# Performance work log

Hardware: AMD Instinct MI355X
Metric: run time of the kernel (lower is better)

The kernel has to match this reference:

```python
import jax, jax.numpy as jnp
import numpy as np

# Config constants (match init_kwargs)
E = 16          # n_routed_experts
G = 4           # n_groups
TOPK_G = 2      # topk_groups
K = 4           # n_activated_experts
ROUTE_SCALE = 2.5446


def setup_inputs() -> dict:
    key = jax.random.key(0)
    ks = jax.random.split(key, 9)
    T, D, H = 2048, 1024, 704
    HS = 2 * H  # shared FFN hidden = n_shared_experts * expert_hidden_dim
    sc = lambda k, shape, fan_in: (jax.random.normal(k, shape, jnp.float32)
                                   * (fan_in ** -0.5))
    return {
        "x":      jax.random.normal(ks[0], (T, D), jnp.float32),
        "gate_w": sc(ks[1], (E, D), D),
        "gate_b": jnp.zeros((E,), jnp.float32),       # V3 routing bias (init 0)
        "w1":     sc(ks[2], (E, H, D), D),            # gate proj per expert
        "w3":     sc(ks[3], (E, H, D), D),            # up proj per expert
        "w2":     sc(ks[4], (E, D, H), H),            # down proj per expert
        "ws1":    sc(ks[5], (HS, D), D),              # shared FFN gate proj
        "ws3":    sc(ks[6], (HS, D), D),              # shared FFN up proj
        "ws2":    sc(ks[7], (D, HS), HS),             # shared FFN down proj
    }


def _gate(x, gate_w, gate_b):
    """DeepSeek-V3 sigmoid gate with bias routing + group-limited masking."""
    T = x.shape[0]
    logits = x @ gate_w.T                                   # [T, E]
    scores = jax.nn.sigmoid(logits).astype(jnp.float32)     # original_scores
    routing = scores + gate_b                               # bias only affects routing
    g = routing.reshape(T, G, E // G)
    # use_bias=True -> group score = sum of top-2 routing scores in group
    group_scores = jnp.sum(jax.lax.top_k(g, 2)[0], axis=-1)     # [T, G]
    top_groups = jax.lax.top_k(group_scores, TOPK_G)[1]         # [T, TOPK_G]
    keep = jnp.any(jnp.arange(G)[None, :, None] == top_groups[:, None, :],
                   axis=-1)                                     # [T, G]
    routing = jnp.where(keep[:, :, None], g, -jnp.inf).reshape(T, E)
    idx = jax.lax.top_k(routing, K)[1]                          # [T, K]
    w = jnp.take_along_axis(scores, idx, axis=1)                # un-biased weights
    w = w / jnp.clip(jnp.sum(w, axis=-1, keepdims=True), 1e-9)  # sigmoid renorm
    w = (w * ROUTE_SCALE).astype(x.dtype)
    return w, idx


def reference(x, gate_w, gate_b, w1, w3, w2, ws1, ws3, ws2):
    T, D = x.shape
    weights, idx = _gate(x, gate_w, gate_b)                 # [T,K], [T,K]
    # Dense dispatch/combine matrix: combine[t, e] = gate weight (0 if unrouted)
    combine = jnp.zeros((T, E), x.dtype).at[
        jnp.arange(T)[:, None], idx].add(weights)           # [T, E]
    # Routed experts: SwiGLU per expert, grouped GEMMs
    hg = jnp.einsum('td,ehd->eth', x, w1)                   # [E, T, H]
    hu = jnp.einsum('td,ehd->eth', x, w3)                   # [E, T, H]
    eo = jnp.einsum('eth,edh->etd', jax.nn.silu(hg) * hu, w2)  # [E, T, D]
    y_routed = jnp.einsum('etd,te->td', eo, combine)        # [T, D]
    # Shared experts (always active SwiGLU)
    y_shared = (jax.nn.silu(x @ ws1.T) * (x @ ws3.T)) @ ws2.T
    return y_routed + y_shared
```

## Files before the change

kernel.cpp:

```cpp
#include <hip/hip_runtime.h>
#include <hip/hip_bf16.h>
#include <math.h>

typedef __attribute__((ext_vector_type(4))) float   f32x4;
typedef __attribute__((ext_vector_type(8))) short   short8;
typedef __attribute__((ext_vector_type(8))) __bf16  bf16x8;

union SB8 { short8 s; bf16x8 b; };

__device__ __forceinline__ short f2bf(float f) {
  union { float f; unsigned u; } v; v.f = f;
  unsigned r = v.u + 0x7fffu + ((v.u >> 16) & 1u);
  return (short)(r >> 16);
}

__device__ __forceinline__ short8 cvt8(f32x4 a, f32x4 b) {
  short8 r;
  r[0] = f2bf(a[0]); r[1] = f2bf(a[1]); r[2] = f2bf(a[2]); r[3] = f2bf(a[3]);
  r[4] = f2bf(b[0]); r[5] = f2bf(b[1]); r[6] = f2bf(b[2]); r[7] = f2bf(b[3]);
  return r;
}

__device__ __forceinline__ void ldsload16(const short* g, short* l) {
  __builtin_amdgcn_global_load_lds(
      (const __attribute__((address_space(1))) unsigned int*)g,
      (__attribute__((address_space(3))) unsigned int*)l, 16, 0, 0);
}

#define TT   2048
#define DD   1024
#define HH   704
#define HSS  1408
#define EE   16
#define CAP  2048

#define O1  2097152ULL
#define O2  13631488ULL
#define O3  25165824ULL
#define O4  36700160ULL
#define O5  38141952ULL
#define O6  39583744ULL
#define CVT_TOTAL 41025536ULL
#define CVT_BLOCKS 5008

__global__ __launch_bounds__(256)
void cvt_gate(const float* __restrict__ x,  const float* __restrict__ w1,
              const float* __restrict__ w3, const float* __restrict__ w2,
              const float* __restrict__ s1, const float* __restrict__ s3,
              const float* __restrict__ s2, short* __restrict__ dst,
              const float* __restrict__ gw, const float* __restrict__ gb,
              int* __restrict__ counts, int* __restrict__ tok,
              float* __restrict__ wgt, int* __restrict__ eslot)
{
  if (blockIdx.x < CVT_BLOCKS) {
    const size_t blk = (size_t)blockIdx.x * 8192;
    #pragma unroll
    for (int k = 0; k < 4; k++) {
      size_t i = blk + (size_t)k * 2048 + (size_t)threadIdx.x * 8;
      const float* src;
      if      (i < O1) src = x  + i;
      else if (i < O2) src = w1 + (i - O1);
      else if (i < O3) src = w3 + (i - O2);
      else if (i < O4) src = w2 + (i - O3);
      else if (i < O5) src = s1 + (i - O4);
      else if (i < O6) src = s3 + (i - O5);
      else             src = s2 + (i - O6);
      f32x4 a = *(const f32x4*)src;
      f32x4 b = *(const f32x4*)(src + 4);
      *(short8*)(dst + i) = cvt8(a, b);
    }
    return;
  }

  const int lane = threadIdx.x & 63;
  const int wid  = threadIdx.x >> 6;
  const int t    = (blockIdx.x - CVT_BLOCKS) * 4 + wid;
  const int e    = lane & 15;
  const int p    = lane >> 4;

  const float* xp = x + (size_t)t * DD + p * 256;
  const float* gp = gw + (size_t)e * DD + p * 256;

  double acc = 0.0;
  #pragma unroll 8
  for (int i = 0; i < 64; i++) {
    f32x4 xa = *(const f32x4*)(xp + i * 4);
    f32x4 ga = *(const f32x4*)(gp + i * 4);
    acc += (double)xa[0] * (double)ga[0];
    acc += (double)xa[1] * (double)ga[1];
    acc += (double)xa[2] * (double)ga[2];
    acc += (double)xa[3] * (double)ga[3];
  }
  acc += __shfl_xor(acc, 16);
  acc += __shfl_xor(acc, 32);
  float accf = (float)acc;

  float lf[EE], sc[EE], r[EE];
  #pragma unroll
  for (int j = 0; j < EE; j++) lf[j] = __shfl(accf, j);
  #pragma unroll
  for (int j = 0; j < EE; j++) {
    sc[j] = 1.f / (1.f + expf(-lf[j]));
    r[j] = sc[j] + gb[j];
  }
  float gs[4];
  #pragma unroll
  for (int g = 0; g < 4; g++) {
    float m1 = -1e30f, m2 = -1e30f;
    #pragma unroll
    for (int j = 0; j < 4; j++) {
      float v = r[g * 4 + j];
      if (v > m1) { m2 = m1; m1 = v; }
      else if (v > m2) { m2 = v; }
    }
    gs[g] = m1 + m2;
  }
  int g1 = 0, g2 = -1; float b1 = -1e30f, b2 = -1e30f;
  #pragma unroll
  for (int g = 0; g < 4; g++) {
    if (gs[g] > b1) { b2 = b1; g2 = g1; b1 = gs[g]; g1 = g; }
    else if (gs[g] > b2) { b2 = gs[g]; g2 = g; }
  }
  int idx[4]; float wv[4]; float wsum = 0.f;
  unsigned used = 0;
  #pragma unroll
  for (int k = 0; k < 4; k++) {
    float best = -1e30f; int bi = 0;
    #pragma unroll
    for (int j = 0; j < EE; j++) {
      int g = j >> 2;
      bool keep = (g == g1) || (g == g2);
      if (keep && !((used >> j) & 1) && r[j] > best) { best = r[j]; bi = j; }
    }
    used |= 1u << bi; idx[k] = bi; wv[k] = sc[bi]; wsum += sc[bi];
  }
  float div = wsum < 1e-9f ? 1e-9f : wsum;
  if (lane < 4) {
    float w = wv[lane] / div * 2.5446f;
    int slot = atomicAdd(&counts[idx[lane]], 1);
    tok[idx[lane] * CAP + slot] = t;
    wgt[idx[lane] * CAP + slot] = w;
    eslot[t * 4 + lane] = (idx[lane] << 16) | slot;
  }
}

__global__ __launch_bounds__(256, 2)
void gemm1_merged(const short* __restrict__ xb, const short* __restrict__ w1b,
                  const short* __restrict__ w3b, const short* __restrict__ ws1b,
                  const short* __restrict__ ws3b, short* __restrict__ act_r,
                  short* __restrict__ act_s, const int* __restrict__ counts,
                  const int* __restrict__ tok)
{
  const int z = blockIdx.z;
  const bool routed = (z < EE);
  const int Mt = blockIdx.y, Nt = blockIdx.x;

  int cnt, N, rowbase = 0;
  const short *W1, *W3;
  short* act;
  if (routed) {
    if (Nt >= 6) return;
    cnt = counts[z];
    if (Mt * 128 >= cnt) return;
    int rb = 0;
    for (int i = 0; i < z; i++) rb += counts[i];
    rowbase = rb;
    N = HH;
    W1 = w1b + (size_t)z * HH * DD;
    W3 = w3b + (size_t)z * HH * DD;
    act = act_r;
  } else {
    cnt = TT; N = HSS; W1 = ws1b; W3 = ws3b; act = act_s;
  }

  __shared__ __align__(16) short lA[128 * 64];
  __shared__ __align__(16) short lB1[128 * 64];
  __shared__ __align__(16) short lB3[128 * 64];

  const int tid = threadIdx.x, lane = tid & 63, wv = tid >> 6;
  const int srow = lane >> 3, schunk = lane & 7, scg = schunk ^ srow;

  const short* pa[4]; const short* pb1[4]; const short* pb3[4];
  #pragma unroll
  for (int i = 0; i < 4; i++) {
    const int g = wv * 4 + i;
    int arow = Mt * 128 + g * 8 + srow;
    if (routed) {
      int slot = arow < cnt ? arow : cnt - 1;
      arow = tok[z * CAP + slot];
    }
    pa[i] = xb + (size_t)arow * DD + scg * 8;
    const int brow = Nt * 128 + g * 8 + srow;
    pb1[i] = W1 + (size_t)brow * DD + scg * 8;
    pb3[i] = W3 + (size_t)brow * DD + scg * 8;
  }

  f32x4 acc1[8][2], acc3[8][2];
  #pragma unroll
  for (int i = 0; i < 8; i++) {
    #pragma unroll
    for (int j = 0; j < 2; j++) { acc1[i][j] = (f32x4)0.f; acc3[i][j] = (f32x4)0.f; }
  }

  const int q = lane >> 4, r7 = lane & 7, hi = (lane & 15) >> 3;

  for (int kk = 0; kk < DD; kk += 64) {
    #pragma unroll
    for (int i = 0; i < 4; i++) {
      const int g = wv * 4 + i;
      ldsload16(pa[i] + kk,  lA  + g * 512);
      ldsload16(pb1[i] + kk, lB1 + g * 512);
      ldsload16(pb3[i] + kk, lB3 + g * 512);
    }
    __syncthreads();
    #pragma unroll
    for (int kc = 0; kc < 2; kc++) {
      const int cx = (kc * 4 + q) ^ r7;
      SB8 b1f[2], b3f[2];
      #pragma unroll
      for (int ntl = 0; ntl < 2; ntl++) {
        const int a16 = ((wv * 2 + ntl) * 2 + hi) * 64 + r7 * 8 + cx;
        b1f[ntl].s = *(const short8*)(lB1 + a16 * 8);
        b3f[ntl].s = *(const short8*)(lB3 + a16 * 8);
      }
      #pragma unroll
      for (int mt = 0; mt < 8; mt++) {
        const int a16 = (2 * mt + hi) * 64 + r7 * 8 + cx;
        SB8 af; af.s = *(const short8*)(lA + a16 * 8);
        acc1[mt][0] = __builtin_amdgcn_mfma_f32_16x16x32_bf16(af.b, b1f[0].b, acc1[mt][0], 0, 0, 0);
        acc1[mt][1] = __builtin_amdgcn_mfma_f32_16x16x32_bf16(af.b, b1f[1].b, acc1[mt][1], 0, 0, 0);
        acc3[mt][0] = __builtin_amdgcn_mfma_f32_16x16x32_bf16(af.b, b3f[0].b, acc3[mt][0], 0, 0, 0);
        acc3[mt][1] = __builtin_amdgcn_mfma_f32_16x16x32_bf16(af.b, b3f[1].b, acc3[mt][1], 0, 0, 0);
      }
    }
    __syncthreads();
  }

  const int quad = lane >> 4, lcol = lane & 15;
  #pragma unroll
  for (int mt = 0; mt < 8; mt++) {
    #pragma unroll
    for (int ntl = 0; ntl < 2; ntl++) {
      const int col = Nt * 128 + (wv * 2 + ntl) * 16 + lcol;
      #pragma unroll
      for (int rg = 0; rg < 4; rg++) {
        const int r = Mt * 128 + mt * 16 + quad * 4 + rg;
        if (r < cnt && col < N) {
          float g = acc1[mt][ntl][rg], u = acc3[mt][ntl][rg];
          float a = g / (1.f + __expf(-g)) * u;
          act[(size_t)(rowbase + r) * N + col] = f2bf(a);
        }
      }
    }
  }
}

__global__ __launch_bounds__(256, 2)
void gemm2_merged(const short* __restrict__ act_r, const short* __restrict__ act_s,
                  const short* __restrict__ w2b, const short* __restrict__ ws2b,
                  float* __restrict__ y, float* __restrict__ outr,
                  const int* __restrict__ counts, const float* __restrict__ wgt)
{
  const int z = blockIdx.z;
  const bool routed = (z < EE);
  const int Mt = blockIdx.y, Nt = blockIdx.x;

  int cnt, Kd, rowbase = 0;
  const short *A, *W;
  if (routed) {
    cnt = counts[z];
    if (Mt * 128 >= cnt) return;
    int rb = 0;
    for (int i = 0; i < z; i++) rb += counts[i];
    rowbase = rb;
    Kd = HH;
    A = act_r + (size_t)rowbase * HH;
    W = w2b + (size_t)z * DD * HH;
  } else {
    cnt = TT; Kd = HSS; A = act_s; W = ws2b;
  }

  __shared__ __align__(16) short lA[128 * 64];
  __shared__ __align__(16) short lB[128 * 64];

  const int tid = threadIdx.x, lane = tid & 63, wv = tid >> 6;
  const int srow = lane >> 3, schunk = lane & 7, scg = schunk ^ srow;

  const short* pa[4]; const short* pb[4];
  #pragma unroll
  for (int i = 0; i < 4; i++) {
    const int g = wv * 4 + i;
    int arow = Mt * 128 + g * 8 + srow;
    if (arow >= cnt) arow = cnt - 1;
    pa[i] = A + (size_t)arow * Kd + scg * 8;
    const int brow = Nt * 128 + g * 8 + srow;
    pb[i] = W + (size_t)brow * Kd + scg * 8;
  }

  f32x4 acc[8][2];
  #pragma unroll
  for (int i = 0; i < 8; i++) { acc[i][0] = (f32x4)0.f; acc[i][1] = (f32x4)0.f; }

  const int q = lane >> 4, r7 = lane & 7, hi = (lane & 15) >> 3;

  for (int kk = 0; kk < Kd; kk += 64) {
    #pragma unroll
    for (int i = 0; i < 4; i++) {
      const int g = wv * 4 + i;
      ldsload16(pa[i] + kk, lA + g * 512);
      ldsload16(pb[i] + kk, lB + g * 512);
    }
    __syncthreads();
    #pragma unroll
    for (int kc = 0; kc < 2; kc++) {
      const int cx = (kc * 4 + q) ^ r7;
      SB8 bf[2];
      #pragma unroll
      for (int ntl = 0; ntl < 2; ntl++) {
        const int a16 = ((wv * 2 + ntl) * 2 + hi) * 64 + r7 * 8 + cx;
        bf[ntl].s = *(const short8*)(lB + a16 * 8);
      }
      #pragma unroll
      for (int mt = 0; mt < 8; mt++) {
        const int a16 = (2 * mt + hi) * 64 + r7 * 8 + cx;
        SB8 af; af.s = *(const short8*)(lA + a16 * 8);
        acc[mt][0] = __builtin_amdgcn_mfma_f32_16x16x32_bf16(af.b, bf[0].b, acc[mt][0], 0, 0, 0);
        acc[mt][1] = __builtin_amdgcn_mfma_f32_16x16x32_bf16(af.b, bf[1].b, acc[mt][1], 0, 0, 0);
      }
    }
    __syncthreads();
  }

  const int quad = lane >> 4, lcol = lane & 15;
  #pragma unroll
  for (int mt = 0; mt < 8; mt++) {
    #pragma unroll
    for (int ntl = 0; ntl < 2; ntl++) {
      const int col = Nt * 128 + (wv * 2 + ntl) * 16 + lcol;
      #pragma unroll
      for (int rg = 0; rg < 4; rg++) {
        const int slot = Mt * 128 + mt * 16 + quad * 4 + rg;
        const float v = acc[mt][ntl][rg];
        if (routed) {
          if (slot < cnt) {
            const float w = wgt[z * CAP + slot];
            outr[(size_t)(rowbase + slot) * DD + col] = w * v;
          }
        } else {
          y[(size_t)slot * DD + col] = v;
        }
      }
    }
  }
}

__global__ __launch_bounds__(256)
void combine_kernel(float* __restrict__ y, const float* __restrict__ outr,
                    const int* __restrict__ eslot, const int* __restrict__ counts)
{
  const int t = blockIdx.x;
  const int d = threadIdx.x * 4;

  int offs[EE];
  int s = 0;
  #pragma unroll
  for (int i = 0; i < EE; i++) { offs[i] = s; s += counts[i]; }

  f32x4 accv = *(f32x4*)(y + (size_t)t * DD + d);
  #pragma unroll
  for (int k = 0; k < 4; k++) {
    const int es = eslot[t * 4 + k];
    const int row = offs[es >> 16] + (es & 0xFFFF);
    accv += *(const f32x4*)(outr + (size_t)row * DD + d);
  }
  *(f32x4*)(y + (size_t)t * DD + d) = accv;
}

extern "C" void kernel_launch(void* const* d_in, const int* in_sizes, int n_in,
                              void* d_out, int out_size, void* d_ws, size_t ws_size,
                              hipStream_t stream) {
  const float* x      = (const float*)d_in[0];
  const float* gate_w = (const float*)d_in[1];
  const float* gate_b = (const float*)d_in[2];
  const float* w1     = (const float*)d_in[3];
  const float* w3     = (const float*)d_in[4];
  const float* w2     = (const float*)d_in[5];
  const float* ws1    = (const float*)d_in[6];
  const float* ws3    = (const float*)d_in[7];
  const float* ws2    = (const float*)d_in[8];
  float* y = (float*)d_out;

  char* ws = (char*)d_ws;
  int*   counts = (int*)ws;
  int*   tok    = (int*)(ws + 1024);
  float* wgt    = (float*)(ws + 1024 + (size_t)EE * CAP * 4);
  int*   eslot  = (int*)(ws + 1024 + (size_t)EE * CAP * 8);
  short* bf     = (short*)(ws + 1024 + (size_t)EE * CAP * 8 + (size_t)TT * 16);
  short* xb   = bf;
  short* w1b  = bf + O1;
  short* w3b  = bf + O2;
  short* w2b  = bf + O3;
  short* ws1b = bf + O4;
  short* ws3b = bf + O5;
  short* ws2b = bf + O6;
  short* act_r = bf + CVT_TOTAL;
  short* act_s = act_r + (size_t)8192 * HH;
  float* outr = (float*)(bf + O1);

  (void)hipMemsetAsync(counts, 0, 256, stream);

  cvt_gate<<<CVT_BLOCKS + TT / 4, 256, 0, stream>>>(
      x, w1, w3, w2, ws1, ws3, ws2, bf,
      gate_w, gate_b, counts, tok, wgt, eslot);

  gemm1_merged<<<dim3(11, TT / 128, EE + 1), 256, 0, stream>>>(
      xb, w1b, w3b, ws1b, ws3b, act_r, act_s, counts, tok);

  gemm2_merged<<<dim3(DD / 128, TT / 128, EE + 1), 256, 0, stream>>>(
      act_r, act_s, w2b, ws2b, y, outr, counts, wgt);

  combine_kernel<<<TT, 256, 0, stream>>>(y, outr, eslot, counts);
}
```

Before: 356.4 us.

## Overlap w2/ws2 bf16 conversion with first GEMM and pad expert counters

Moves the fp32-to-bf16 conversion of the down-projection weights (w2, ws2) out of the first kernel and into an extra z-slice of the gate/up GEMM launch, so that conversion can overlap with GEMM work. The gate blocks are now placed first in the first kernel, and the conversion loop issues all loads before any converts. Expert counters are padded to 32-int stride to avoid atomic contention on a shared cache line, and the double-precision gate dot product uses four accumulators to shorten the dependency chain. The trade-off is that the z=0 conversion blocks share the GPU with GEMM blocks and may delay scheduling of GEMM tiles.

Result: faster. 317.9 us (-10.8%).

```diff
diff --git a/kernel.cpp b/kernel.cpp
--- a/kernel.cpp
+++ b/kernel.cpp
@@ -33,6 +33,7 @@
 #define HSS  1408
 #define EE   16
 #define CAP  2048
+#define CSTR 32
 
 #define O1  2097152ULL
 #define O2  13631488ULL
@@ -41,56 +42,70 @@
 #define O5  38141952ULL
 #define O6  39583744ULL
 #define CVT_TOTAL 41025536ULL
-#define CVT_BLOCKS 5008
+
+#define W2SZ    11534336ULL
+#define WS1SZ   1441792ULL
+#define WS1END  26607616ULL
+#define CVTA_TOTAL  28049408ULL
+#define CVTA_BLOCKS 3424
+#define GATE_BLOCKS 512
 
 __global__ __launch_bounds__(256)
-void cvt_gate(const float* __restrict__ x,  const float* __restrict__ w1,
-              const float* __restrict__ w3, const float* __restrict__ w2,
-              const float* __restrict__ s1, const float* __restrict__ s3,
-              const float* __restrict__ s2, short* __restrict__ dst,
+void gate_cvt(const float* __restrict__ x,  const float* __restrict__ w1,
+              const float* __restrict__ w3, const float* __restrict__ s1,
+              const float* __restrict__ s3, short* __restrict__ dst,
               const float* __restrict__ gw, const float* __restrict__ gb,
               int* __restrict__ counts, int* __restrict__ tok,
               float* __restrict__ wgt, int* __restrict__ eslot)
 {
-  if (blockIdx.x < CVT_BLOCKS) {
-    const size_t blk = (size_t)blockIdx.x * 8192;
+  if (blockIdx.x >= GATE_BLOCKS) {
+    const int tid = threadIdx.x;
+    const size_t base = (size_t)(blockIdx.x - GATE_BLOCKS) * 8192;
+    const float* sp[4]; short* dp[4];
     #pragma unroll
     for (int k = 0; k < 4; k++) {
-      size_t i = blk + (size_t)k * 2048 + (size_t)threadIdx.x * 8;
-      const float* src;
-      if      (i < O1) src = x  + i;
-      else if (i < O2) src = w1 + (i - O1);
-      else if (i < O3) src = w3 + (i - O2);
-      else if (i < O4) src = w2 + (i - O3);
-      else if (i < O5) src = s1 + (i - O4);
-      else if (i < O6) src = s3 + (i - O5);
-      else             src = s2 + (i - O6);
-      f32x4 a = *(const f32x4*)src;
-      f32x4 b = *(const f32x4*)(src + 4);
-      *(short8*)(dst + i) = cvt8(a, b);
-    }
+      const size_t sb = base + (size_t)k * 2048;
+      const float* src; size_t doff;
+      if      (sb < O1)     { src = x  + sb;            doff = sb; }
+      else if (sb < O2)     { src = w1 + (sb - O1);     doff = sb; }
+      else if (sb < O3)     { src = w3 + (sb - O2);     doff = sb; }
+      else if (sb < WS1END) { src = s1 + (sb - O3);     doff = sb + W2SZ; }
+      else                  { src = s3 + (sb - WS1END); doff = sb + W2SZ; }
+      sp[k] = src + tid * 8;
+      dp[k] = dst + doff + tid * 8;
+    }
+    f32x4 va[8];
+    #pragma unroll
+    for (int k = 0; k < 4; k++) {
+      va[2 * k]     = *(const f32x4*)(sp[k]);
+      va[2 * k + 1] = *(const f32x4*)(sp[k] + 4);
+    }
+    #pragma unroll
+    for (int k = 0; k < 4; k++)
+      *(short8*)(dp[k]) = cvt8(va[2 * k], va[2 * k + 1]);
     return;
   }
 
   const int lane = threadIdx.x & 63;
   const int wid  = threadIdx.x >> 6;
-  const int t    = (blockIdx.x - CVT_BLOCKS) * 4 + wid;
+  const int t    = blockIdx.x * 4 + wid;
   const int e    = lane & 15;
   const int p    = lane >> 4;
 
   const float* xp = x + (size_t)t * DD + p * 256;
   const float* gp = gw + (size_t)e * DD + p * 256;
 
-  double acc = 0.0;
+  double a0 = 0.0, a1 = 0.0, a2 = 0.0, a3 = 0.0;
   #pragma unroll 8
   for (int i = 0; i < 64; i++) {
     f32x4 xa = *(const f32x4*)(xp + i * 4);
     f32x4 ga = *(const f32x4*)(gp + i * 4);
-    acc += (double)xa[0] * (double)ga[0];
-    acc += (double)xa[1] * (double)ga[1];
-    acc += (double)xa[2] * (double)ga[2];
-    acc += (double)xa[3] * (double)ga[3];
-  }
+    a0 += (double)xa[0] * (double)ga[0];
+    a1 += (double)xa[1] * (double)ga[1];
+    a2 += (double)xa[2] * (double)ga[2];
+    a3 += (double)xa[3] * (double)ga[3];
+  }
+  double acc = (a0 + a1) + (a2 + a3);
   acc += __shfl_xor(acc, 16);
   acc += __shfl_xor(acc, 32);
   float accf = (float)acc;
@@ -137,7 +152,7 @@
   float div = wsum < 1e-9f ? 1e-9f : wsum;
   if (lane < 4) {
     float w = wv[lane] / div * 2.5446f;
-    int slot = atomicAdd(&counts[idx[lane]], 1);
+    int slot = atomicAdd(&counts[idx[lane] * CSTR], 1);
     tok[idx[lane] * CAP + slot] = t;
     wgt[idx[lane] * CAP + slot] = w;
     eslot[t * 4 + lane] = (idx[lane] << 16) | slot;
@@ -149,25 +164,60 @@
                   const short* __restrict__ w3b, const short* __restrict__ ws1b,
                   const short* __restrict__ ws3b, short* __restrict__ act_r,
                   short* __restrict__ act_s, const int* __restrict__ counts,
-                  const int* __restrict__ tok)
+                  const int* __restrict__ tok,
+                  const float* __restrict__ w2f, const float* __restrict__ ws2f,
+                  short* __restrict__ w2bd, short* __restrict__ ws2bd)
 {
   const int z = blockIdx.z;
-  const bool routed = (z < EE);
   const int Mt = blockIdx.y, Nt = blockIdx.x;
+
+  if (z == 0) {
+    const int bid = Mt * 11 + Nt;
+    const int tid = threadIdx.x;
+    for (int s = 0; s < 9; s++) {
+      const size_t base = (size_t)bid * 73728 + (size_t)s * 8192;
+      const float* sp[4]; short* dp[4];
+      #pragma unroll
+      for (int k = 0; k < 4; k++) {
+        const size_t sb = base + (size_t)k * 2048;
+        if (sb < W2SZ) {
+          sp[k] = w2f + sb + tid * 8;
+          dp[k] = w2bd + sb + tid * 8;
+        } else {
+          const size_t o = sb - W2SZ;
+          sp[k] = ws2f + o + tid * 8;
+          dp[k] = ws2bd + o + tid * 8;
+        }
+      }
+      f32x4 va[8];
+      #pragma unroll
+      for (int k = 0; k < 4; k++) {
+        va[2 * k]     = *(const f32x4*)(sp[k]);
+        va[2 * k + 1] = *(const f32x4*)(sp[k] + 4);
+      }
+      #pragma unroll
+      for (int k = 0; k < 4; k++)
+        *(short8*)(dp[k]) = cvt8(va[2 * k], va[2 * k + 1]);
+    }
+    return;
+  }
+
+  const bool routed = (z <= EE);
+  const int e = z - 1;
 
   int cnt, N, rowbase = 0;
   const short *W1, *W3;
   short* act;
   if (routed) {
     if (Nt >= 6) return;
-    cnt = counts[z];
+    cnt = counts[e * CSTR];
     if (Mt * 128 >= cnt) return;
     int rb = 0;
-    for (int i = 0; i < z; i++) rb += counts[i];
+    for (int i = 0; i < e; i++) rb += counts[i * CSTR];
     rowbase = rb;
     N = HH;
-    W1 = w1b + (size_t)z * HH * DD;
-    W3 = w3b + (size_t)z * HH * DD;
+    W1 = w1b + (size_t)e * HH * DD;
+    W3 = w3b + (size_t)e * HH * DD;
     act = act_r;
   } else {
     cnt = TT; N = HSS; W1 = ws1b; W3 = ws3b; act = act_s;
@@ -187,7 +237,7 @@
     int arow = Mt * 128 + g * 8 + srow;
     if (routed) {
       int slot = arow < cnt ? arow : cnt - 1;
-      arow = tok[z * CAP + slot];
+      arow = tok[e * CAP + slot];
     }
     pa[i] = xb + (size_t)arow * DD + scg * 8;
     const int brow = Nt * 128 + g * 8 + srow;
@@ -268,10 +318,10 @@
   int cnt, Kd, rowbase = 0;
   const short *A, *W;
   if (routed) {
-    cnt = counts[z];
+    cnt = counts[z * CSTR];
     if (Mt * 128 >= cnt) return;
     int rb = 0;
-    for (int i = 0; i < z; i++) rb += counts[i];
+    for (int i = 0; i < z; i++) rb += counts[i * CSTR];
     rowbase = rb;
     Kd = HH;
     A = act_r + (size_t)rowbase * HH;
@@ -364,7 +414,7 @@
   int offs[EE];
   int s = 0;
   #pragma unroll
-  for (int i = 0; i < EE; i++) { offs[i] = s; s += counts[i]; }
+  for (int i = 0; i < EE; i++) { offs[i] = s; s += counts[i * CSTR]; }
 
   f32x4 accv = *(f32x4*)(y + (size_t)t * DD + d);
   #pragma unroll
@@ -392,10 +442,10 @@
 
   char* ws = (char*)d_ws;
   int*   counts = (int*)ws;
-  int*   tok    = (int*)(ws + 1024);
-  float* wgt    = (float*)(ws + 1024 + (size_t)EE * CAP * 4);
-  int*   eslot  = (int*)(ws + 1024 + (size_t)EE * CAP * 8);
-  short* bf     = (short*)(ws + 1024 + (size_t)EE * CAP * 8 + (size_t)TT * 16);
+  int*   tok    = (int*)(ws + 2048);
+  float* wgt    = (float*)(ws + 2048 + (size_t)EE * CAP * 4);
+  int*   eslot  = (int*)(ws + 2048 + (size_t)EE * CAP * 8);
+  short* bf     = (short*)(ws + 2048 + (size_t)EE * CAP * 8 + (size_t)TT * 16);
   short* xb   = bf;
   short* w1b  = bf + O1;
   short* w3b  = bf + O2;
@@ -407,14 +457,15 @@
   short* act_s = act_r + (size_t)8192 * HH;
   float* outr = (float*)(bf + O1);
 
-  (void)hipMemsetAsync(counts, 0, 256, stream);
-
-  cvt_gate<<<CVT_BLOCKS + TT / 4, 256, 0, stream>>>(
-      x, w1, w3, w2, ws1, ws3, ws2, bf,
+  (void)hipMemsetAsync(counts, 0, EE * CSTR * sizeof(int), stream);
+
+  gate_cvt<<<GATE_BLOCKS + CVTA_BLOCKS, 256, 0, stream>>>(
+      x, w1, w3, ws1, ws3, bf,
       gate_w, gate_b, counts, tok, wgt, eslot);
 
-  gemm1_merged<<<dim3(11, TT / 128, EE + 1), 256, 0, stream>>>(
-      xb, w1b, w3b, ws1b, ws3b, act_r, act_s, counts, tok);
+  gemm1_merged<<<dim3(11, TT / 128, EE + 2), 256, 0, stream>>>(
+      xb, w1b, w3b, ws1b, ws3b, act_r, act_s, counts, tok,
+      w2, ws2, w2b, ws2b);
 
   gemm2_merged<<<dim3(DD / 128, TT / 128, EE + 1), 256, 0, stream>>>(
       act_r, act_s, w2b, ws2b, y, outr, counts, wgt);
```
